# Kernel optimization log

Hardware: AMD Instinct MI355X
Metric: run time of the kernel (lower is better)

Reference implementation:

```python
import jax, jax.numpy as jnp
import numpy as np

N = 50000      # nodes
E = 800000     # unique directed edges (avg degree 16)
F = 64         # input_dim
D = 64         # output_dim (== F -> residual is identity)
ALPHA = 0.5
LCS_THR = 0.5  # enable_lcs_masking=True, lcs_threshold=0.5


def setup_inputs() -> dict:
    key = jax.random.key(0)
    ks = jax.random.split(key, 16)
    x = jax.random.normal(ks[0], (N, F), jnp.float32)
    src = jax.random.randint(ks[1], (E,), 0, N, jnp.int32)
    dst = jax.random.randint(ks[2], (E,), 0, N, jnp.int32)
    # integer-valued multiplicities in {1,2,3,4} (recurring-transaction counts)
    counts = jnp.floor(jax.random.uniform(ks[3], (E,), jnp.float32) * 4.0) + 1.0
    def lin(k, fan_in, shape):
        return jax.random.normal(k, shape, jnp.float32) / np.float32(np.sqrt(fan_in))
    return dict(
        x=x, counts=counts,
        W_s2d=lin(ks[4], F, (F, D)), b_s2d=jnp.zeros((D,), jnp.float32),
        W_d2s=lin(ks[5], F, (F, D)), b_d2s=jnp.zeros((D,), jnp.float32),
        W_l1=lin(ks[6], 2 * F, (2 * F, F)), b_l1=jnp.zeros((F,), jnp.float32),
        W_l2=lin(ks[7], F, (F, 1)), b_l2=jnp.zeros((1,), jnp.float32),
        W_g1=lin(ks[8], 2 * D, (2 * D, D)), b_g1=jnp.zeros((D,), jnp.float32),
        W_g2=lin(ks[9], D, (D, 1)), b_g2=jnp.zeros((1,), jnp.float32),
        src=src, dst=dst,
    )


def reference(x, counts, W_s2d, b_s2d, W_d2s, b_d2s,
              W_l1, b_l1, W_l2, b_l2, W_g1, b_g1, W_g2, b_g2,
              src, dst):
    # in/out degrees from full (unmasked) multiplicities, clamped at 1
    in_deg = jnp.maximum(jax.ops.segment_sum(counts, dst, num_segments=N), 1.0)
    out_deg = jnp.maximum(jax.ops.segment_sum(counts, src, num_segments=N), 1.0)

    # LCS per unique edge: sigmoid(MLP([x_src, x_dst])), detached in torch
    lcs_in = jnp.concatenate([x[src], x[dst]], axis=-1)          # [E, 2F]
    lcs = jax.nn.sigmoid(
        jax.nn.relu(lcs_in @ W_l1 + b_l1) @ W_l2 + b_l2)[:, 0]   # [E]
    lcs = jax.lax.stop_gradient(lcs)
    keep = (lcs >= LCS_THR).astype(x.dtype)                      # LCS masking

    # symmetric-normalized edge weights with multiplicity counts
    w = counts * keep * jax.lax.rsqrt(out_deg[src] * in_deg[dst])  # [E]

    # direction-aware message passing (redundancy-eliminated, per unique edge)
    h_s2d = x @ W_s2d + b_s2d                                    # [N, D]
    h_d2s = x @ W_d2s + b_d2s                                    # [N, D]
    m_in = jax.ops.segment_sum(w[:, None] * h_s2d[src], dst, num_segments=N)
    m_out = jax.ops.segment_sum(w[:, None] * h_d2s[dst], src, num_segments=N)

    # node-wise gating over inbound vs outbound flows
    gate = jax.nn.sigmoid(
        jax.nn.relu(jnp.concatenate([m_in, m_out], axis=-1) @ W_g1 + b_g1)
        @ W_g2 + b_g2)                                           # [N, 1]

    # gated alpha-blend + identity residual (input_dim == output_dim)
    out = ALPHA * gate * m_in + (1.0 - ALPHA) * (1.0 - gate) * m_out + x
    return out
```

## Files before the change

### kernel.cpp

```cpp
#include <hip/hip_runtime.h>
#include <math.h>


typedef unsigned long long u64;

#define SLOTS 56

__device__ __forceinline__ float bflo(unsigned u) { return __uint_as_float(u << 16); }
__device__ __forceinline__ float bfhi(unsigned u) { return __uint_as_float(u & 0xffff0000u); }
__device__ __forceinline__ unsigned rne16(float f) {
    unsigned u = __float_as_uint(f);
    return (u + 0x7fffu + ((u >> 16) & 1u)) >> 16;
}

__global__ __launch_bounds__(256) void proj_zero_kernel(
    const float* __restrict__ x,
    const float* __restrict__ Wl1,  const float* __restrict__ bl1,
    const float* __restrict__ Ws2d, const float* __restrict__ bs2d,
    const float* __restrict__ Wd2s, const float* __restrict__ bd2s,
    const float* __restrict__ Wg1,  float* __restrict__ Wg1q,
    float* __restrict__ A, float* __restrict__ B,
    unsigned* __restrict__ Ah, unsigned* __restrict__ Bh,
    unsigned* __restrict__ HSh, unsigned* __restrict__ HDh,
    int4* __restrict__ zp4, int nz4, int PB, int N)
{
    if (blockIdx.x >= PB) {
        if (blockIdx.x == PB + 64) {
            for (int i = threadIdx.x; i < 8192; i += 256) {
                const int k = i >> 6, c = i & 63;
                Wg1q[((k >> 2) * 64 + c) * 4 + (k & 3)] = Wg1[i];
            }
            return;
        }
        const int t0 = (blockIdx.x - PB) * 256 + threadIdx.x;
        const int stride = 64 * 256;
        const int4 z = make_int4(0, 0, 0, 0);
        for (int i = t0; i < nz4; i += stride) zp4[i] = z;
        return;
    }
    __shared__ float xs[64][64];
    const int tid = threadIdx.x;
    const int n0  = blockIdx.x * 64;
    const int wv  = tid >> 6;
    const int cc  = tid & 63;

    const float* Wbase; const float* bias; float* obase; unsigned* obh;
    switch (wv) {
        case 0:  Wbase = Wl1;           bias = bl1;     obase = A;       obh = Ah;  break;
        case 1:  Wbase = Wl1 + 64 * 64; bias = nullptr; obase = B;       obh = Bh;  break;
        case 2:  Wbase = Ws2d;          bias = bs2d;    obase = nullptr; obh = HSh; break;
        default: Wbase = Wd2s;          bias = bd2s;    obase = nullptr; obh = HDh; break;
    }

    float wr[64];
#pragma unroll
    for (int k = 0; k < 64; ++k) wr[k] = Wbase[k * 64 + cc];
    const float bv = bias ? bias[cc] : 0.f;

#pragma unroll
    for (int j = 0; j < 4; ++j) {
        int f4  = tid + j * 256;
        int row = f4 >> 4;
        int c4  = f4 & 15;
        int gn  = n0 + row;
        float4 v = (gn < N) ? ((const float4*)x)[(long)gn * 16 + c4]
                            : make_float4(0.f, 0.f, 0.f, 0.f);
        ((float4*)&xs[row][0])[c4] = v;
    }
    __syncthreads();

    const int nmax = (N - n0 < 64) ? (N - n0) : 64;
    for (int n = 0; n < nmax; ++n) {
        float acc = bv;
#pragma unroll
        for (int k = 0; k < 64; k += 4) {
            float4 xv = *((const float4*)&xs[n][k]);
            acc += xv.x * wr[k] + xv.y * wr[k + 1] + xv.z * wr[k + 2] + xv.w * wr[k + 3];
        }
        if (obase) obase[(long)(n0 + n) * 64 + cc] = acc;
        const float part = __shfl_xor(acc, 1);
        if ((cc & 1) == 0)
            obh[(long)(n0 + n) * 32 + (cc >> 1)] = (rne16(part) << 16) | rne16(acc);
    }
}

#define LCS_MARGIN 0.04f
__global__ __launch_bounds__(256) void edge_w_kernel(
    const int* __restrict__ src, const int* __restrict__ dst,
    const float* __restrict__ counts,
    const float* __restrict__ A, const float* __restrict__ B,
    const unsigned* __restrict__ Ah, const unsigned* __restrict__ Bh,
    const float* __restrict__ Wl2, const float* __restrict__ bl2,
    u64* __restrict__ pk, unsigned* __restrict__ rec, int N, int E)
{
    const int tid = threadIdx.x;
    const int e   = blockIdx.x * 32 + (tid >> 3);
    const int c   = tid & 7;
    if (e >= E) return;

    const int s = src[e];
    const int d = dst[e];
    const uint4  ua  = *((const uint4*)(Ah + (long)s * 32 + c * 4));
    const uint4  ub  = *((const uint4*)(Bh + (long)d * 32 + c * 4));
    const float4 wl0 = *((const float4*)(Wl2 + c * 8));
    const float4 wl1 = *((const float4*)(Wl2 + c * 8 + 4));

    float p = fmaxf(bflo(ua.x) + bflo(ub.x), 0.f) * wl0.x
            + fmaxf(bfhi(ua.x) + bfhi(ub.x), 0.f) * wl0.y
            + fmaxf(bflo(ua.y) + bflo(ub.y), 0.f) * wl0.z
            + fmaxf(bfhi(ua.y) + bfhi(ub.y), 0.f) * wl0.w
            + fmaxf(bflo(ua.z) + bflo(ub.z), 0.f) * wl1.x
            + fmaxf(bfhi(ua.z) + bfhi(ub.z), 0.f) * wl1.y
            + fmaxf(bflo(ua.w) + bflo(ub.w), 0.f) * wl1.z
            + fmaxf(bfhi(ua.w) + bfhi(ub.w), 0.f) * wl1.w;
    p += __shfl_xor(p, 1); p += __shfl_xor(p, 2); p += __shfl_xor(p, 4);

    float z = p + bl2[0];
    if (fabsf(z) < LCS_MARGIN) {
        const float4 a0 = *((const float4*)(A + (long)s * 64 + c * 8));
        const float4 a1 = *((const float4*)(A + (long)s * 64 + c * 8 + 4));
        const float4 b0 = *((const float4*)(B + (long)d * 64 + c * 8));
        const float4 b1 = *((const float4*)(B + (long)d * 64 + c * 8 + 4));
        float q = fmaxf(a0.x + b0.x, 0.f) * wl0.x + fmaxf(a0.y + b0.y, 0.f) * wl0.y
                + fmaxf(a0.z + b0.z, 0.f) * wl0.z + fmaxf(a0.w + b0.w, 0.f) * wl0.w
                + fmaxf(a1.x + b1.x, 0.f) * wl1.x + fmaxf(a1.y + b1.y, 0.f) * wl1.y
                + fmaxf(a1.z + b1.z, 0.f) * wl1.z + fmaxf(a1.w + b1.w, 0.f) * wl1.w;
        q += __shfl_xor(q, 1); q += __shfl_xor(q, 2); q += __shfl_xor(q, 4);
        z = q + bl2[0];
    }

    if (c == 0) {
        const u64 keep = (z >= 0.f) ? 1ull : 0ull;
        const unsigned ic = (unsigned)__float2int_rn(counts[e]);
        const u64 od = atomicAdd(pk + d,     (keep << 32) | (u64)ic);
        const u64 os = atomicAdd(pk + N + s, (keep << 32) | (u64)ic);
        if (keep) {
            rec[(long)d * SLOTS + (int)(od >> 32)]       = ((unsigned)s << 16) | ic;
            rec[(long)(N + s) * SLOTS + (int)(os >> 32)] = ((unsigned)d << 16) | ic;
        }
    }
}

__global__ __launch_bounds__(256) void gather_gate_kernel(
    const u64* __restrict__ pk, const unsigned* __restrict__ rec,
    const unsigned* __restrict__ HSh, const unsigned* __restrict__ HDh,
    const float* __restrict__ x,
    const float* __restrict__ Wg1q, const float* __restrict__ bg1,
    const float* __restrict__ Wg2, const float* __restrict__ bg2,
    float* __restrict__ out, int N)
{
    __shared__ float mbuf[4][128];
    const int tid  = threadIdx.x;
    const int wv   = tid >> 6;
    const int lane = tid & 63;
    const int g    = lane >> 3;
    const int c    = lane & 7;
    const int n    = blockIdx.x * 4 + wv;
    if (n >= N) return;

    const unsigned* pklo = (const unsigned*)pk;

    const u64 pin  = pk[n];
    const u64 pout = pk[N + n];
    const int ei = (int)(pin >> 32);
    const int eo = (int)(pout >> 32);
    const float qin  = 1.f / sqrtf(fmaxf((float)(unsigned)pin,  1.f));
    const float qout = 1.f / sqrtf(fmaxf((float)(unsigned)pout, 1.f));
    const unsigned* rin  = rec + (long)n * SLOTS;
    const unsigned* rout = rec + (long)(N + n) * SLOTS;

    float mi[8], mo[8];
#pragma unroll
    for (int j = 0; j < 8; ++j) { mi[j] = 0.f; mo[j] = 0.f; }

    int ii = g, jo = g;
    while ((ii < ei) || (jo < eo)) {
        const bool pa = ii < ei;
        const bool pb = jo < eo;
        const unsigned ra = rin[pa ? ii : 0];
        const unsigned rb = rout[pb ? jo : 0];
        const unsigned sa = ra >> 16;
        const unsigned sb = rb >> 16;
        const float dga = (float)pklo[2 * (N + (int)sa)];
        const float dgb = (float)pklo[2 * (int)sb];
        const float wa = pa ? (float)(ra & 0xFFu) * (1.f / sqrtf(fmaxf(dga, 1.f))) : 0.f;
        const float wb = pb ? (float)(rb & 0xFFu) * (1.f / sqrtf(fmaxf(dgb, 1.f))) : 0.f;
        const uint4 ua = *((const uint4*)(HSh + (long)sa * 32 + c * 4));
        const uint4 ub = *((const uint4*)(HDh + (long)sb * 32 + c * 4));
        mi[0] += wa * bflo(ua.x);  mo[0] += wb * bflo(ub.x);
        mi[1] += wa * bfhi(ua.x);  mo[1] += wb * bfhi(ub.x);
        mi[2] += wa * bflo(ua.y);  mo[2] += wb * bflo(ub.y);
        mi[3] += wa * bfhi(ua.y);  mo[3] += wb * bfhi(ub.y);
        mi[4] += wa * bflo(ua.z);  mo[4] += wb * bflo(ub.z);
        mi[5] += wa * bfhi(ua.z);  mo[5] += wb * bfhi(ub.z);
        mi[6] += wa * bflo(ua.w);  mo[6] += wb * bflo(ub.w);
        mi[7] += wa * bfhi(ua.w);  mo[7] += wb * bfhi(ub.w);
        ii += 8; jo += 8;
    }

#pragma unroll
    for (int j = 0; j < 8; ++j) {
        mi[j] += __shfl_xor(mi[j], 8);
        mi[j] += __shfl_xor(mi[j], 16);
        mi[j] += __shfl_xor(mi[j], 32);
        mo[j] += __shfl_xor(mo[j], 8);
        mo[j] += __shfl_xor(mo[j], 16);
        mo[j] += __shfl_xor(mo[j], 32);
    }
    if (g == 0) {
#pragma unroll
        for (int j = 0; j < 8; ++j) {
            mbuf[wv][c * 8 + j]      = mi[j] * qin;
            mbuf[wv][64 + c * 8 + j] = mo[j] * qout;
        }
    }

    float acc = bg1[lane];
    const float* mb = &mbuf[wv][0];
#pragma unroll 8
    for (int k4 = 0; k4 < 32; ++k4) {
        const float4 m4 = ((const float4*)mb)[k4];
        const float4 w4 = ((const float4*)Wg1q)[k4 * 64 + lane];
        acc += m4.x * w4.x + m4.y * w4.y + m4.z * w4.z + m4.w * w4.w;
    }
    float v = fmaxf(acc, 0.f) * Wg2[lane];
    v += __shfl_xor(v, 1);  v += __shfl_xor(v, 2);  v += __shfl_xor(v, 4);
    v += __shfl_xor(v, 8);  v += __shfl_xor(v, 16); v += __shfl_xor(v, 32);

    const float gate = 1.f / (1.f + expf(-(v + bg2[0])));
    const float miv = mb[lane];
    const float mov = mb[64 + lane];
    out[(long)n * 64 + lane] = 0.5f * gate * miv + 0.5f * (1.f - gate) * mov
                             + x[(long)n * 64 + lane];
}

extern "C" void kernel_launch(void* const* d_in, const int* in_sizes, int n_in,
                              void* d_out, int out_size, void* d_ws, size_t ws_size,
                              hipStream_t stream) {
    const float* x      = (const float*)d_in[0];
    const float* counts = (const float*)d_in[1];
    const float* Ws2d   = (const float*)d_in[2];
    const float* bs2d   = (const float*)d_in[3];
    const float* Wd2s   = (const float*)d_in[4];
    const float* bd2s   = (const float*)d_in[5];
    const float* Wl1    = (const float*)d_in[6];
    const float* bl1    = (const float*)d_in[7];
    const float* Wl2    = (const float*)d_in[8];
    const float* bl2    = (const float*)d_in[9];
    const float* Wg1    = (const float*)d_in[10];
    const float* bg1    = (const float*)d_in[11];
    const float* Wg2    = (const float*)d_in[12];
    const float* bg2    = (const float*)d_in[13];
    const int*   src    = (const int*)d_in[14];
    const int*   dst    = (const int*)d_in[15];

    const int N  = in_sizes[0] / 64;
    const int E  = in_sizes[14];
    const int PB = (N + 63) / 64;

    float* ws      = (float*)d_ws;
    float* Wg1q    = ws;
    float* A       = ws + 8192;
    float* B       = A + 64L * N;
    unsigned* Ah   = (unsigned*)(B + 64L * N);
    unsigned* Bh   = Ah + 32L * N;
    unsigned* HSh  = Bh + 32L * N;
    unsigned* HDh  = HSh + 32L * N;
    u64* pk        = (u64*)(HDh + 32L * N);
    unsigned* rec  = (unsigned*)(pk + 2L * N);

    proj_zero_kernel<<<PB + 65, 256, 0, stream>>>(
        x, Wl1, bl1, Ws2d, bs2d, Wd2s, bd2s, Wg1, Wg1q,
        A, B, Ah, Bh, HSh, HDh, (int4*)pk, N, PB, N);

    edge_w_kernel<<<(E + 31) / 32, 256, 0, stream>>>(
        src, dst, counts, A, B, Ah, Bh, Wl2, bl2, pk, rec, N, E);

    gather_gate_kernel<<<(N + 3) / 4, 256, 0, stream>>>(
        pk, rec, HSh, HDh, x, Wg1q, bg1, Wg2, bg2, (float*)d_out, N);
}
```

Measured before the change: 279.2 us.

## Process two edges per thread group and prescale projections by source degree

```diff
diff --git a/kernel.cpp b/kernel.cpp
--- a/kernel.cpp
+++ b/kernel.cpp
@@ -94,51 +94,106 @@
     u64* __restrict__ pk, unsigned* __restrict__ rec, int N, int E)
 {
     const int tid = threadIdx.x;
-    const int e   = blockIdx.x * 32 + (tid >> 3);
+    const int e0  = blockIdx.x * 64 + (tid >> 3) * 2;
     const int c   = tid & 7;
-    if (e >= E) return;
-
-    const int s = src[e];
-    const int d = dst[e];
-    const uint4  ua  = *((const uint4*)(Ah + (long)s * 32 + c * 4));
-    const uint4  ub  = *((const uint4*)(Bh + (long)d * 32 + c * 4));
+    if (e0 >= E) return;
+    const bool two = (e0 + 1) < E;
+    const int e1 = two ? e0 + 1 : e0;
+
+    const int s0 = src[e0], d0 = dst[e0];
+    const int s1 = src[e1], d1 = dst[e1];
+    const uint4 ua0 = *((const uint4*)(Ah + (long)s0 * 32 + c * 4));
+    const uint4 ub0 = *((const uint4*)(Bh + (long)d0 * 32 + c * 4));
+    const uint4 ua1 = *((const uint4*)(Ah + (long)s1 * 32 + c * 4));
+    const uint4 ub1 = *((const uint4*)(Bh + (long)d1 * 32 + c * 4));
     const float4 wl0 = *((const float4*)(Wl2 + c * 8));
     const float4 wl1 = *((const float4*)(Wl2 + c * 8 + 4));
 
-    float p = fmaxf(bflo(ua.x) + bflo(ub.x), 0.f) * wl0.x
-            + fmaxf(bfhi(ua.x) + bfhi(ub.x), 0.f) * wl0.y
-            + fmaxf(bflo(ua.y) + bflo(ub.y), 0.f) * wl0.z
-            + fmaxf(bfhi(ua.y) + bfhi(ub.y), 0.f) * wl0.w
-            + fmaxf(bflo(ua.z) + bflo(ub.z), 0.f) * wl1.x
-            + fmaxf(bfhi(ua.z) + bfhi(ub.z), 0.f) * wl1.y
-            + fmaxf(bflo(ua.w) + bflo(ub.w), 0.f) * wl1.z
-            + fmaxf(bfhi(ua.w) + bfhi(ub.w), 0.f) * wl1.w;
-    p += __shfl_xor(p, 1); p += __shfl_xor(p, 2); p += __shfl_xor(p, 4);
-
-    float z = p + bl2[0];
-    if (fabsf(z) < LCS_MARGIN) {
-        const float4 a0 = *((const float4*)(A + (long)s * 64 + c * 8));
-        const float4 a1 = *((const float4*)(A + (long)s * 64 + c * 8 + 4));
-        const float4 b0 = *((const float4*)(B + (long)d * 64 + c * 8));
-        const float4 b1 = *((const float4*)(B + (long)d * 64 + c * 8 + 4));
-        float q = fmaxf(a0.x + b0.x, 0.f) * wl0.x + fmaxf(a0.y + b0.y, 0.f) * wl0.y
-                + fmaxf(a0.z + b0.z, 0.f) * wl0.z + fmaxf(a0.w + b0.w, 0.f) * wl0.w
-                + fmaxf(a1.x + b1.x, 0.f) * wl1.x + fmaxf(a1.y + b1.y, 0.f) * wl1.y
-                + fmaxf(a1.z + b1.z, 0.f) * wl1.z + fmaxf(a1.w + b1.w, 0.f) * wl1.w;
-        q += __shfl_xor(q, 1); q += __shfl_xor(q, 2); q += __shfl_xor(q, 4);
-        z = q + bl2[0];
+    float p0 = fmaxf(bflo(ua0.x) + bflo(ub0.x), 0.f) * wl0.x
+             + fmaxf(bfhi(ua0.x) + bfhi(ub0.x), 0.f) * wl0.y
+             + fmaxf(bflo(ua0.y) + bflo(ub0.y), 0.f) * wl0.z
+             + fmaxf(bfhi(ua0.y) + bfhi(ub0.y), 0.f) * wl0.w
+             + fmaxf(bflo(ua0.z) + bflo(ub0.z), 0.f) * wl1.x
+             + fmaxf(bfhi(ua0.z) + bfhi(ub0.z), 0.f) * wl1.y
+             + fmaxf(bflo(ua0.w) + bflo(ub0.w), 0.f) * wl1.z
+             + fmaxf(bfhi(ua0.w) + bfhi(ub0.w), 0.f) * wl1.w;
+    float p1 = fmaxf(bflo(ua1.x) + bflo(ub1.x), 0.f) * wl0.x
+             + fmaxf(bfhi(ua1.x) + bfhi(ub1.x), 0.f) * wl0.y
+             + fmaxf(bflo(ua1.y) + bflo(ub1.y), 0.f) * wl0.z
+             + fmaxf(bfhi(ua1.y) + bfhi(ub1.y), 0.f) * wl0.w
+             + fmaxf(bflo(ua1.z) + bflo(ub1.z), 0.f) * wl1.x
+             + fmaxf(bfhi(ua1.z) + bfhi(ub1.z), 0.f) * wl1.y
+             + fmaxf(bflo(ua1.w) + bflo(ub1.w), 0.f) * wl1.z
+             + fmaxf(bfhi(ua1.w) + bfhi(ub1.w), 0.f) * wl1.w;
+    p0 += __shfl_xor(p0, 1); p1 += __shfl_xor(p1, 1);
+    p0 += __shfl_xor(p0, 2); p1 += __shfl_xor(p1, 2);
+    p0 += __shfl_xor(p0, 4); p1 += __shfl_xor(p1, 4);
+
+    const float bl = bl2[0];
+    float z0 = p0 + bl;
+    float z1 = p1 + bl;
+    if (fmaxf(-fabsf(z0), -fabsf(z1)) > -LCS_MARGIN) {
+        const float4 a00 = *((const float4*)(A + (long)s0 * 64 + c * 8));
+        const float4 a01 = *((const float4*)(A + (long)s0 * 64 + c * 8 + 4));
+        const float4 b00 = *((const float4*)(B + (long)d0 * 64 + c * 8));
+        const float4 b01 = *((const float4*)(B + (long)d0 * 64 + c * 8 + 4));
+        float q0 = fmaxf(a00.x + b00.x, 0.f) * wl0.x + fmaxf(a00.y + b00.y, 0.f) * wl0.y
+                 + fmaxf(a00.z + b00.z, 0.f) * wl0.z + fmaxf(a00.w + b00.w, 0.f) * wl0.w
+                 + fmaxf(a01.x + b01.x, 0.f) * wl1.x + fmaxf(a01.y + b01.y, 0.f) * wl1.y
+                 + fmaxf(a01.z + b01.z, 0.f) * wl1.z + fmaxf(a01.w + b01.w, 0.f) * wl1.w;
+        const float4 a10 = *((const float4*)(A + (long)s1 * 64 + c * 8));
+        const float4 a11 = *((const float4*)(A + (long)s1 * 64 + c * 8 + 4));
+        const float4 b10 = *((const float4*)(B + (long)d1 * 64 + c * 8));
+        const float4 b11 = *((const float4*)(B + (long)d1 * 64 + c * 8 + 4));
+        float q1 = fmaxf(a10.x + b10.x, 0.f) * wl0.x + fmaxf(a10.y + b10.y, 0.f) * wl0.y
+                 + fmaxf(a10.z + b10.z, 0.f) * wl0.z + fmaxf(a10.w + b10.w, 0.f) * wl0.w
+                 + fmaxf(a11.x + b11.x, 0.f) * wl1.x + fmaxf(a11.y + b11.y, 0.f) * wl1.y
+                 + fmaxf(a11.z + b11.z, 0.f) * wl1.z + fmaxf(a11.w + b11.w, 0.f) * wl1.w;
+        q0 += __shfl_xor(q0, 1); q1 += __shfl_xor(q1, 1);
+        q0 += __shfl_xor(q0, 2); q1 += __shfl_xor(q1, 2);
+        q0 += __shfl_xor(q0, 4); q1 += __shfl_xor(q1, 4);
+        if (fabsf(z0) < LCS_MARGIN) z0 = q0 + bl;
+        if (fabsf(z1) < LCS_MARGIN) z1 = q1 + bl;
     }
 
     if (c == 0) {
-        const u64 keep = (z >= 0.f) ? 1ull : 0ull;
-        const unsigned ic = (unsigned)__float2int_rn(counts[e]);
-        const u64 od = atomicAdd(pk + d,     (keep << 32) | (u64)ic);
-        const u64 os = atomicAdd(pk + N + s, (keep << 32) | (u64)ic);
-        if (keep) {
-            rec[(long)d * SLOTS + (int)(od >> 32)]       = ((unsigned)s << 16) | ic;
-            rec[(long)(N + s) * SLOTS + (int)(os >> 32)] = ((unsigned)d << 16) | ic;
-        }
-    }
+        {
+            const u64 keep = (z0 >= 0.f) ? 1ull : 0ull;
+            const unsigned ic = (unsigned)__float2int_rn(counts[e0]);
+            const u64 od = atomicAdd(pk + d0,     (keep << 32) | (u64)ic);
+            const u64 os = atomicAdd(pk + N + s0, (keep << 32) | (u64)ic);
+            if (keep) {
+                rec[(long)d0 * SLOTS + (int)(od >> 32)]       = ((unsigned)s0 << 16) | ic;
+                rec[(long)(N + s0) * SLOTS + (int)(os >> 32)] = ((unsigned)d0 << 16) | ic;
+            }
+        }
+        if (two) {
+            const u64 keep = (z1 >= 0.f) ? 1ull : 0ull;
+            const unsigned ic = (unsigned)__float2int_rn(counts[e1]);
+            const u64 od = atomicAdd(pk + d1,     (keep << 32) | (u64)ic);
+            const u64 os = atomicAdd(pk + N + s1, (keep << 32) | (u64)ic);
+            if (keep) {
+                rec[(long)d1 * SLOTS + (int)(od >> 32)]       = ((unsigned)s1 << 16) | ic;
+                rec[(long)(N + s1) * SLOTS + (int)(os >> 32)] = ((unsigned)d1 << 16) | ic;
+            }
+        }
+    }
+}
+
+__global__ __launch_bounds__(256) void rescale_kernel(
+    const u64* __restrict__ pk, unsigned* __restrict__ HSh, unsigned* __restrict__ HDh,
+    int N)
+{
+    const int idx = blockIdx.x * 256 + threadIdx.x;
+    if (idx >= 64 * N) return;
+    const bool isS = idx < 32 * N;
+    const int i = isS ? idx : idx - 32 * N;
+    const int node = i >> 5;
+    unsigned* H = isS ? HSh : HDh;
+    const u64 pv = pk[isS ? (N + node) : node];
+    const float isq = 1.f / sqrtf(fmaxf((float)(unsigned)pv, 1.f));
+    const unsigned u = H[i];
+    H[i] = (rne16(bfhi(u) * isq) << 16) | rne16(bflo(u) * isq);
 }
 
 __global__ __launch_bounds__(256) void gather_gate_kernel(
@@ -158,8 +213,6 @@
     const int n    = blockIdx.x * 4 + wv;
     if (n >= N) return;
 
-    const unsigned* pklo = (const unsigned*)pk;
-
     const u64 pin  = pk[n];
     const u64 pout = pk[N + n];
     const int ei = (int)(pin >> 32);
@@ -181,10 +234,8 @@
         const unsigned rb = rout[pb ? jo : 0];
         const unsigned sa = ra >> 16;
         const unsigned sb = rb >> 16;
-        const float dga = (float)pklo[2 * (N + (int)sa)];
-        const float dgb = (float)pklo[2 * (int)sb];
-        const float wa = pa ? (float)(ra & 0xFFu) * (1.f / sqrtf(fmaxf(dga, 1.f))) : 0.f;
-        const float wb = pb ? (float)(rb & 0xFFu) * (1.f / sqrtf(fmaxf(dgb, 1.f))) : 0.f;
+        const float wa = pa ? (float)(ra & 0xFFu) : 0.f;
+        const float wb = pb ? (float)(rb & 0xFFu) : 0.f;
         const uint4 ua = *((const uint4*)(HSh + (long)sa * 32 + c * 4));
         const uint4 ub = *((const uint4*)(HDh + (long)sb * 32 + c * 4));
         mi[0] += wa * bflo(ua.x);  mo[0] += wb * bflo(ub.x);
@@ -273,8 +324,10 @@
         x, Wl1, bl1, Ws2d, bs2d, Wd2s, bd2s, Wg1, Wg1q,
         A, B, Ah, Bh, HSh, HDh, (int4*)pk, N, PB, N);
 
-    edge_w_kernel<<<(E + 31) / 32, 256, 0, stream>>>(
+    edge_w_kernel<<<(E + 63) / 64, 256, 0, stream>>>(
         src, dst, counts, A, B, Ah, Bh, Wl2, bl2, pk, rec, N, E);
+
+    rescale_kernel<<<(64 * N + 255) / 256, 256, 0, stream>>>(pk, HSh, HDh, N);
 
     gather_gate_kernel<<<(N + 3) / 4, 256, 0, stream>>>(
         pk, rec, HSh, HDh, x, Wg1q, bg1, Wg2, bg2, (float*)d_out, N);
```

Result: no change. 283.3 us (+1.5%).
